# Kernel tuning notes

Measured on AMD Instinct MI355X. Metric: run time of the kernel, lower is better.

## Reference

```python
import jax, jax.numpy as jnp
import numpy as np

B, T, C, D = 8, 4096, 1024, 128  # batch, seq (=block_size), dim_embd, head_features

def setup_inputs() -> dict:
    key = jax.random.key(0)
    k1, k2, k3, k4 = jax.random.split(key, 4)
    s = 0.02
    return {
        "x": jax.random.normal(k1, (B, T, C), dtype=jnp.float32),
        "wq": jax.random.normal(k2, (C, D), dtype=jnp.float32) * s,
        "wk": jax.random.normal(k3, (C, D), dtype=jnp.float32) * s,
        "wv": jax.random.normal(k4, (C, D), dtype=jnp.float32) * s,
    }

def reference(x, wq, wk, wv):
    # q,k,v: [B,T,D]
    q = jnp.einsum('btc,cd->btd', x, wq)
    k = jnp.einsum('btc,cd->btd', x, wk)
    v = jnp.einsum('btc,cd->btd', x, wv)
    scale = k.shape[-1] ** -0.5
    wei = jnp.einsum('bqd,bkd->bqk', q, k) * scale  # [B,T,T]
    causal = jnp.tril(jnp.ones((T, T), dtype=bool))
    wei = jnp.where(causal, wei, -jnp.inf)
    attn = jax.nn.softmax(wei, axis=-1)  # dropout p=0.0 -> identity
    out = jnp.einsum('bqk,bkd->bqd', attn, v)  # [B,T,D]
    return out
```

## Files before the change

kernel.cpp:

```cpp
#include <hip/hip_runtime.h>

#define TT 4096
#define CC 1024
#define DD 128

typedef __attribute__((ext_vector_type(8))) short s16x8;
typedef __attribute__((ext_vector_type(4))) short s16x4;
typedef __attribute__((ext_vector_type(8))) __bf16 bf16x8;
typedef __attribute__((ext_vector_type(4))) float f32x4;
typedef __attribute__((ext_vector_type(2))) float f32x2;

__device__ __forceinline__ short f2bf(float f) {
    union { float f; unsigned u; } v; v.f = f;
    unsigned r = v.u + 0x7fffu + ((v.u >> 16) & 1u);
    return (short)(r >> 16);
}

__device__ __forceinline__ unsigned cvt_pk(float lo, float hi) {
    unsigned r;
    asm("v_cvt_pk_bf16_f32 %0, %1, %2" : "=v"(r) : "v"(lo), "v"(hi));
    return r;
}

__device__ __forceinline__ f32x4 mfma16(s16x8 a, s16x8 b, f32x4 c) {
    return __builtin_amdgcn_mfma_f32_16x16x32_bf16(
        __builtin_bit_cast(bf16x8, a), __builtin_bit_cast(bf16x8, b), c, 0, 0, 0);
}

__device__ __forceinline__ void gload_lds16(const short* g, short* l) {
    __builtin_amdgcn_global_load_lds(
        (const __attribute__((address_space(1))) void*)g,
        (__attribute__((address_space(3))) void*)l, 16, 0, 0);
}

__global__ void wt_kernel(const float* __restrict__ wq, const float* __restrict__ wk,
                          const float* __restrict__ wv, short* __restrict__ wT) {
    int idx = blockIdx.x * 256 + threadIdx.x;
    int d = idx & 127;
    int c = (idx >> 7) & 1023;
    int wsel = idx >> 17;
    const float* w = (wsel == 0) ? wq : (wsel == 1) ? wk : wv;
    float v = w[(size_t)c * DD + d];
    if (wsel == 0) v *= 0.08838834764831845f * 1.4426950408889634f;
    wT[(size_t)wsel * DD * CC + (size_t)d * CC + c] = f2bf(v);
}

__global__ __launch_bounds__(512)
void qkv_kernel(const float* __restrict__ x, const short* __restrict__ wT,
                short* __restrict__ qo, short* __restrict__ ko, short* __restrict__ vTo) {
    __shared__ short lw[2][384 * 64];
    const int mt = blockIdx.x;
    const int tid = threadIdx.x, lane = tid & 63, wid = tid >> 6;
    const int l15 = lane & 15, g = lane >> 4;
    const int wm = wid >> 1, wn = wid & 1;
    const int arow = mt * 128 + wm * 32 + l15;
    const float* xr0 = x + (size_t)arow * CC + g * 8;
    const float* xr1 = xr0 + (size_t)16 * CC;

    const f32x4 fz = {0.f, 0.f, 0.f, 0.f};
    f32x4 acc[2][12];
#pragma unroll
    for (int mr = 0; mr < 2; mr++)
#pragma unroll
        for (int nr = 0; nr < 12; nr++) acc[mr][nr] = fz;

    const int swr = wid * 48;
    const short* wsrc = wT + (size_t)(swr + (lane >> 3)) * CC + (lane & 7) * 8;

    float4 pa[2][2][2];
#define LOADA(kc) do { \
    _Pragma("unroll") for (int mr_ = 0; mr_ < 2; mr_++) \
    _Pragma("unroll") for (int ks_ = 0; ks_ < 2; ks_++) { \
        const float* p_ = (mr_ ? xr1 : xr0) + (kc) * 64 + ks_ * 32; \
        pa[mr_][ks_][0] = *(const float4*)p_; \
        pa[mr_][ks_][1] = *(const float4*)(p_ + 4); } \
} while (0)
#define STAGEW(kc, buf) do { \
    _Pragma("unroll") for (int j_ = 0; j_ < 6; j_++) \
        gload_lds16(wsrc + (size_t)(j_ * 8) * CC + (kc) * 64, &lw[buf][(swr + j_ * 8) * 64]); \
} while (0)

    LOADA(0);
    STAGEW(0, 0);
    asm volatile("s_waitcnt vmcnt(0)" ::: "memory");
    __builtin_amdgcn_s_barrier();
    int cur = 0;

    for (int kc = 0; kc < 16; kc++) {
        s16x8 af[2][2];
#pragma unroll
        for (int mr = 0; mr < 2; mr++)
#pragma unroll
            for (int ks = 0; ks < 2; ks++) {
                union { unsigned u[4]; s16x8 v; } cv;
                cv.u[0] = cvt_pk(pa[mr][ks][0].x, pa[mr][ks][0].y);
                cv.u[1] = cvt_pk(pa[mr][ks][0].z, pa[mr][ks][0].w);
                cv.u[2] = cvt_pk(pa[mr][ks][1].x, pa[mr][ks][1].y);
                cv.u[3] = cvt_pk(pa[mr][ks][1].z, pa[mr][ks][1].w);
                af[mr][ks] = cv.v;
            }
        if (kc < 15) { LOADA(kc + 1); STAGEW(kc + 1, cur ^ 1); }
        __builtin_amdgcn_s_setprio(1);
#pragma unroll
        for (int ks = 0; ks < 2; ks++)
#pragma unroll
            for (int nr = 0; nr < 12; nr++) {
                const s16x8 bfg = *(const s16x8*)
                    &lw[cur][(wn * 192 + nr * 16 + l15) * 64 + ks * 32 + g * 8];
                acc[0][nr] = mfma16(af[0][ks], bfg, acc[0][nr]);
                acc[1][nr] = mfma16(af[1][ks], bfg, acc[1][nr]);
            }
        __builtin_amdgcn_s_setprio(0);
        asm volatile("s_waitcnt vmcnt(0) lgkmcnt(0)" ::: "memory");
        __builtin_amdgcn_s_barrier();
        cur ^= 1;
    }

    const int bidx = mt >> 5;
    const int tb = (mt & 31) * 128 + wm * 32;
#pragma unroll
    for (int mr = 0; mr < 2; mr++)
#pragma unroll
        for (int nr = 0; nr < 12; nr++) {
            const int n = wn * 192 + nr * 16 + l15;
            if (n < 256) {
                short* dst; int d;
                if (n < 128) { dst = qo; d = n; } else { dst = ko; d = n - 128; }
#pragma unroll
                for (int i = 0; i < 4; i++) {
                    int t = tb + mr * 16 + g * 4 + i;
                    dst[((size_t)bidx * TT + t) * DD + d] = f2bf(acc[mr][nr][i]);
                }
            } else {
                const int d = n - 256;
                const int t = tb + mr * 16 + g * 4;
                uint2 u;
                u.x = cvt_pk(acc[mr][nr][0], acc[mr][nr][1]);
                u.y = cvt_pk(acc[mr][nr][2], acc[mr][nr][3]);
                *(uint2*)(vTo + ((size_t)bidx * DD + d) * TT + t) = u;
            }
        }
}

__device__ __forceinline__ void attn_stage(const short* kT, const short* vT, int kv0,
                                           short* lkb, short* lvb, int wid, int lane) {
#pragma unroll
    for (int j = 0; j < 4; j++) {
        int rbk = wid * 16 + j * 4;
        int rk = rbk + (lane >> 4);
        int ck = (lane & 15) ^ (rk & 7);
        gload_lds16(kT + (size_t)(kv0 + rk) * DD + ck * 8, lkb + rbk * 128);
        int rbv = wid * 32 + j * 8;
        int dv = rbv + (lane >> 3);
        int cv = (lane & 7) ^ (dv & 7);
        gload_lds16(vT + (size_t)dv * TT + kv0 + cv * 8, lvb + rbv * 64);
    }
}

__global__ __launch_bounds__(256)
void attn_kernel(const short* __restrict__ qb, const short* __restrict__ kb,
                 const short* __restrict__ vb, float* __restrict__ out,
                 float* __restrict__ opart, float* __restrict__ mlpart) {
    const int id = blockIdx.x;
    const int b  = id & 7;
    const int r3 = id >> 3;
    const int qt = r3 & 63;
    const int c  = r3 >> 6;
    const int t0 = c * 16;
    if (t0 > qt) return;
    const int t1 = (t0 + 16 < qt + 1) ? t0 + 16 : qt + 1;
    const int nc = (qt >> 4) + 1;

    __shared__ short lk[2][64 * 128];
    __shared__ short lv[2][128 * 64];
    __shared__ short lp[4][1024];
    const int tid = threadIdx.x, lane = tid & 63, wid = tid >> 6;
    const int l15 = lane & 15, g = lane >> 4;
    const int wq0 = qt * 64 + wid * 16;
    const short* kT = kb + (size_t)b * TT * DD;
    const short* vT = vb + (size_t)b * DD * TT;
    char* lpw = (char*)&lp[wid][0];
    const f32x4 fz = {0.f, 0.f, 0.f, 0.f};

    s16x8 qf[4];
    {
        const short* qp = qb + ((size_t)b * TT + wq0 + l15) * DD + g * 8;
#pragma unroll
        for (int ks = 0; ks < 4; ks++) qf[ks] = *(const s16x8*)(qp + ks * 32);
    }
    f32x4 o[8];
#pragma unroll
    for (int n = 0; n < 8; n++) o[n] = fz;
    float rmax = -1e30f, rsum = 0.f;

    attn_stage(kT, vT, t0 * 64, lk[0], lv[0], wid, lane);
    asm volatile("s_waitcnt vmcnt(0)" ::: "memory");
    __builtin_amdgcn_s_barrier();
    int cur = 0;

    for (int t = t0; t < t1; t++) {
        if (t + 1 < t1) attn_stage(kT, vT, (t + 1) * 64, lk[cur ^ 1], lv[cur ^ 1], wid, lane);
        const int kv0 = t * 64;
        const char* lkc = (const char*)&lk[cur][0];
        const char* lvc = (const char*)&lv[cur][0];

        f32x4 s[4];
        __builtin_amdgcn_s_setprio(1);
#pragma unroll
        for (int sub = 0; sub < 4; sub++) {
            f32x4 a = fz;
#pragma unroll
            for (int ks = 0; ks < 4; ks++) {
                int row = sub * 16 + l15;
                int byte = (row * 256 + ks * 64 + g * 16) ^ ((row & 7) << 4);
                s16x8 kf = *(const s16x8*)(lkc + byte);
                a = mfma16(kf, qf[ks], a);
            }
            s[sub] = a;
        }
        __builtin_amdgcn_s_setprio(0);
        if (t == qt) {
#pragma unroll
            for (int sub = 0; sub < 4; sub++)
#pragma unroll
                for (int i = 0; i < 4; i++) {
                    int k = kv0 + sub * 16 + 4 * g + i;
                    if (k > wq0 + l15) s[sub][i] = -1e30f;
                }
        }
        float m0 = s[0][0];
#pragma unroll
        for (int sub = 0; sub < 4; sub++)
#pragma unroll
            for (int i = 0; i < 4; i++) m0 = fmaxf(m0, s[sub][i]);
        m0 = fmaxf(m0, __shfl_xor(m0, 16));
        m0 = fmaxf(m0, __shfl_xor(m0, 32));
        float mnew = fmaxf(rmax, m0);
        float scal = exp2f(rmax - mnew);
        rmax = mnew;
        float ls = 0.f;
#pragma unroll
        for (int sub = 0; sub < 4; sub++)
#pragma unroll
            for (int i = 0; i < 4; i++) {
                float pv = exp2f(s[sub][i] - mnew);
                s[sub][i] = pv;
                ls += pv;
            }
        ls += __shfl_xor(ls, 16);
        ls += __shfl_xor(ls, 32);
        rsum = rsum * scal + ls;
#pragma unroll
        for (int sub = 0; sub < 4; sub++) {
            uint2 w01;
            w01.x = cvt_pk(s[sub][0], s[sub][1]);
            w01.y = cvt_pk(s[sub][2], s[sub][3]);
            int byte = (l15 * 128 + sub * 32 + g * 8) ^ ((l15 & 7) << 4);
            *(uint2*)(lpw + byte) = w01;
        }
#pragma unroll
        for (int n = 0; n < 8; n++)
#pragma unroll
            for (int i = 0; i < 4; i++) o[n][i] *= scal;
        __builtin_amdgcn_s_setprio(1);
#pragma unroll
        for (int ks2 = 0; ks2 < 2; ks2++) {
            int pbyte = (l15 * 128 + ks2 * 64 + g * 16) ^ ((l15 & 7) << 4);
            s16x8 pf = *(const s16x8*)(lpw + pbyte);
#pragma unroll
            for (int n = 0; n < 8; n++) {
                int vrow = n * 16 + l15;
                int vbyte = (vrow * 128 + ks2 * 64 + g * 16) ^ ((vrow & 7) << 4);
                s16x8 vf = *(const s16x8*)(lvc + vbyte);
                o[n] = mfma16(vf, pf, o[n]);
            }
        }
        __builtin_amdgcn_s_setprio(0);
        asm volatile("s_waitcnt vmcnt(0) lgkmcnt(0)" ::: "memory");
        __builtin_amdgcn_s_barrier();
        cur ^= 1;
    }

    const int r = wid * 16 + l15;
    if (nc == 1) {
        float inv = 1.0f / rsum;
        float* orow = out + ((size_t)b * TT + qt * 64 + r) * DD;
#pragma unroll
        for (int n = 0; n < 8; n++) {
            f32x4 w;
            w[0] = o[n][0] * inv; w[1] = o[n][1] * inv;
            w[2] = o[n][2] * inv; w[3] = o[n][3] * inv;
            __builtin_nontemporal_store(w, (f32x4*)(orow + n * 16 + 4 * g));
        }
    } else {
        const size_t pb = ((size_t)b * 48 + (qt - 16)) * 4 + c;
        float* prow = opart + pb * (64 * 128) + (size_t)r * 128;
#pragma unroll
        for (int n = 0; n < 8; n++) {
            __builtin_nontemporal_store(o[n], (f32x4*)(prow + n * 16 + 4 * g));
        }
        if (g == 0) {
            f32x2 s2; s2[0] = rmax; s2[1] = rsum;
            __builtin_nontemporal_store(s2, (f32x2*)(mlpart + (pb * 64 + r) * 2));
        }
    }
}

__global__ __launch_bounds__(256)
void comb_kernel(const float* __restrict__ opart, const float* __restrict__ mlpart,
                 float* __restrict__ out) {
    const int qtm = blockIdx.x;
    const int b = blockIdx.y;
    const int qt = 16 + qtm;
    const int nc = (qt >> 4) + 1;
    const int tid = threadIdx.x;
    const int row = tid >> 2, quad = tid & 3;
    const size_t base = ((size_t)b * 48 + qtm) * 4;

    float M = -3e38f;
    for (int cc = 0; cc < nc; cc++)
        M = fmaxf(M, mlpart[((base + cc) * 64 + row) * 2]);

    float acc[32];
#pragma unroll
    for (int k = 0; k < 32; k++) acc[k] = 0.f;
    float L = 0.f;
    for (int cc = 0; cc < nc; cc++) {
        float sm = mlpart[((base + cc) * 64 + row) * 2];
        float sl = mlpart[((base + cc) * 64 + row) * 2 + 1];
        float wgt = exp2f(sm - M);
        L += wgt * sl;
        const float* src = opart + (base + cc) * (64 * 128) + (size_t)row * 128 + quad * 32;
#pragma unroll
        for (int k = 0; k < 8; k++) {
            f32x4 v = __builtin_nontemporal_load((const f32x4*)(src + k * 4));
            acc[k * 4 + 0] += wgt * v[0];
            acc[k * 4 + 1] += wgt * v[1];
            acc[k * 4 + 2] += wgt * v[2];
            acc[k * 4 + 3] += wgt * v[3];
        }
    }
    float inv = 1.0f / L;
    float* dst = out + ((size_t)b * TT + qt * 64 + row) * DD + quad * 32;
#pragma unroll
    for (int k = 0; k < 8; k++) {
        f32x4 w;
        w[0] = acc[k * 4 + 0] * inv; w[1] = acc[k * 4 + 1] * inv;
        w[2] = acc[k * 4 + 2] * inv; w[3] = acc[k * 4 + 3] * inv;
        __builtin_nontemporal_store(w, (f32x4*)(dst + k * 4));
    }
}

extern "C" void kernel_launch(void* const* d_in, const int* in_sizes, int n_in,
                              void* d_out, int out_size, void* d_ws, size_t ws_size,
                              hipStream_t stream) {
    const float* x  = (const float*)d_in[0];
    const float* wq = (const float*)d_in[1];
    const float* wk = (const float*)d_in[2];
    const float* wv = (const float*)d_in[3];
    float* out = (float*)d_out;
    char* ws = (char*)d_ws;
    short* wT = (short*)ws;
    short* qb = (short*)(ws + 786432);
    short* kb = (short*)(ws + 786432 + 8388608);
    short* vb = (short*)(ws + 786432 + 16777216);
    float* opart = (float*)(ws + 786432 + 25165824);
    float* mlpart = (float*)(ws + 786432 + 25165824 + 50331648);

    wt_kernel<<<1536, 256, 0, stream>>>(wq, wk, wv, wT);
    qkv_kernel<<<256, 512, 0, stream>>>(x, wT, qb, kb, vb);
    attn_kernel<<<2048, 256, 0, stream>>>(qb, kb, vb, out, opart, mlpart);
    comb_kernel<<<dim3(48, 8), 256, 0, stream>>>(opart, mlpart, out);
}
```

Baseline: 195.4 us.

## Double query rows per attention block and single-buffer K/V with split-phase loads

```diff
diff --git a/kernel.cpp b/kernel.cpp
--- a/kernel.cpp
+++ b/kernel.cpp
@@ -142,166 +142,196 @@
         }
 }
 
-__device__ __forceinline__ void attn_stage(const short* kT, const short* vT, int kv0,
-                                           short* lkb, short* lvb, int wid, int lane) {
-#pragma unroll
-    for (int j = 0; j < 4; j++) {
-        int rbk = wid * 16 + j * 4;
-        int rk = rbk + (lane >> 4);
-        int ck = (lane & 15) ^ (rk & 7);
-        gload_lds16(kT + (size_t)(kv0 + rk) * DD + ck * 8, lkb + rbk * 128);
-        int rbv = wid * 32 + j * 8;
-        int dv = rbv + (lane >> 3);
-        int cv = (lane & 7) ^ (dv & 7);
-        gload_lds16(vT + (size_t)dv * TT + kv0 + cv * 8, lvb + rbv * 64);
-    }
-}
-
 __global__ __launch_bounds__(256)
 void attn_kernel(const short* __restrict__ qb, const short* __restrict__ kb,
                  const short* __restrict__ vb, float* __restrict__ out,
                  float* __restrict__ opart, float* __restrict__ mlpart) {
     const int id = blockIdx.x;
     const int b  = id & 7;
-    const int r3 = id >> 3;
-    const int qt = r3 & 63;
-    const int c  = r3 >> 6;
+    const int Q  = (id >> 3) & 31;
+    const int c  = id >> 8;
     const int t0 = c * 16;
-    if (t0 > qt) return;
-    const int t1 = (t0 + 16 < qt + 1) ? t0 + 16 : qt + 1;
-    const int nc = (qt >> 4) + 1;
-
-    __shared__ short lk[2][64 * 128];
-    __shared__ short lv[2][128 * 64];
-    __shared__ short lp[4][1024];
+    const int tend = 2 * Q + 2;
+    if (t0 >= tend) return;
+    const int t1 = (t0 + 16 < tend) ? t0 + 16 : tend;
+    const int nc = (tend + 15) >> 4;
+
+    __shared__ short lk[64 * 128];
+    __shared__ short lv[128 * 64];
+    __shared__ short lp[4][2048];
     const int tid = threadIdx.x, lane = tid & 63, wid = tid >> 6;
     const int l15 = lane & 15, g = lane >> 4;
-    const int wq0 = qt * 64 + wid * 16;
+    const int wq0 = Q * 128 + wid * 32;
+    const int tqw = wq0 >> 6;
     const short* kT = kb + (size_t)b * TT * DD;
     const short* vT = vb + (size_t)b * DD * TT;
     char* lpw = (char*)&lp[wid][0];
     const f32x4 fz = {0.f, 0.f, 0.f, 0.f};
 
-    s16x8 qf[4];
+    s16x8 qf0[4], qf1[4];
     {
-        const short* qp = qb + ((size_t)b * TT + wq0 + l15) * DD + g * 8;
-#pragma unroll
-        for (int ks = 0; ks < 4; ks++) qf[ks] = *(const s16x8*)(qp + ks * 32);
-    }
-    f32x4 o[8];
-#pragma unroll
-    for (int n = 0; n < 8; n++) o[n] = fz;
-    float rmax = -1e30f, rsum = 0.f;
-
-    attn_stage(kT, vT, t0 * 64, lk[0], lv[0], wid, lane);
+        const short* qp0 = qb + ((size_t)b * TT + wq0 + l15) * DD + g * 8;
+        const short* qp1 = qp0 + 16 * DD;
+#pragma unroll
+        for (int ks = 0; ks < 4; ks++) {
+            qf0[ks] = *(const s16x8*)(qp0 + ks * 32);
+            qf1[ks] = *(const s16x8*)(qp1 + ks * 32);
+        }
+    }
+    f32x4 o0[8], o1[8];
+#pragma unroll
+    for (int n = 0; n < 8; n++) { o0[n] = fz; o1[n] = fz; }
+    float rmax0 = -1e30f, rsum0 = 0.f, rmax1 = -1e30f, rsum1 = 0.f;
+
+#define SK(kv0) do { \
+    _Pragma("unroll") for (int j_ = 0; j_ < 4; j_++) { \
+        int rbk = wid * 16 + j_ * 4; \
+        int rk = rbk + (lane >> 4); \
+        int ck = (lane & 15) ^ (rk & 7); \
+        gload_lds16(kT + (size_t)((kv0) + rk) * DD + ck * 8, lk + rbk * 128); } \
+} while (0)
+#define SV(kv0) do { \
+    _Pragma("unroll") for (int j_ = 0; j_ < 4; j_++) { \
+        int rbv = wid * 32 + j_ * 8; \
+        int dv = rbv + (lane >> 3); \
+        int cv = (lane & 7) ^ (dv & 7); \
+        gload_lds16(vT + (size_t)dv * TT + (kv0) + cv * 8, lv + rbv * 64); } \
+} while (0)
+
+    SK(t0 * 64);
+    SV(t0 * 64);
     asm volatile("s_waitcnt vmcnt(0)" ::: "memory");
     __builtin_amdgcn_s_barrier();
-    int cur = 0;
 
     for (int t = t0; t < t1; t++) {
-        if (t + 1 < t1) attn_stage(kT, vT, (t + 1) * 64, lk[cur ^ 1], lv[cur ^ 1], wid, lane);
         const int kv0 = t * 64;
-        const char* lkc = (const char*)&lk[cur][0];
-        const char* lvc = (const char*)&lv[cur][0];
-
-        f32x4 s[4];
-        __builtin_amdgcn_s_setprio(1);
-#pragma unroll
-        for (int sub = 0; sub < 4; sub++) {
-            f32x4 a = fz;
-#pragma unroll
-            for (int ks = 0; ks < 4; ks++) {
-                int row = sub * 16 + l15;
-                int byte = (row * 256 + ks * 64 + g * 16) ^ ((row & 7) << 4);
-                s16x8 kf = *(const s16x8*)(lkc + byte);
-                a = mfma16(kf, qf[ks], a);
-            }
-            s[sub] = a;
-        }
-        __builtin_amdgcn_s_setprio(0);
-        if (t == qt) {
+        const int tn = (t + 1 < 63) ? t + 1 : 63;
+        asm volatile("s_waitcnt vmcnt(4)" ::: "memory");
+        f32x4 s0[4], s1[4];
+        if (t <= tqw) {
+            __builtin_amdgcn_s_setprio(1);
+#pragma unroll
+            for (int sub = 0; sub < 4; sub++) {
+                f32x4 a0 = fz, a1 = fz;
+#pragma unroll
+                for (int ks = 0; ks < 4; ks++) {
+                    int row = sub * 16 + l15;
+                    int byte = (row * 256 + ks * 64 + g * 16) ^ ((row & 7) << 4);
+                    s16x8 kf = *(const s16x8*)((const char*)lk + byte);
+                    a0 = mfma16(kf, qf0[ks], a0);
+                    a1 = mfma16(kf, qf1[ks], a1);
+                }
+                s0[sub] = a0; s1[sub] = a1;
+            }
+            __builtin_amdgcn_s_setprio(0);
+        }
+        __builtin_amdgcn_s_barrier();
+        SK(tn * 64);
+        if (t <= tqw) {
+            if (t == tqw) {
+#pragma unroll
+                for (int sub = 0; sub < 4; sub++)
+#pragma unroll
+                    for (int i = 0; i < 4; i++) {
+                        int k = kv0 + sub * 16 + 4 * g + i;
+                        if (k > wq0 + l15) s0[sub][i] = -1e30f;
+                        if (k > wq0 + 16 + l15) s1[sub][i] = -1e30f;
+                    }
+            }
+            float m0 = s0[0][0], m1 = s1[0][0];
 #pragma unroll
             for (int sub = 0; sub < 4; sub++)
 #pragma unroll
                 for (int i = 0; i < 4; i++) {
-                    int k = kv0 + sub * 16 + 4 * g + i;
-                    if (k > wq0 + l15) s[sub][i] = -1e30f;
+                    m0 = fmaxf(m0, s0[sub][i]);
+                    m1 = fmaxf(m1, s1[sub][i]);
                 }
-        }
-        float m0 = s[0][0];
-#pragma unroll
-        for (int sub = 0; sub < 4; sub++)
-#pragma unroll
-            for (int i = 0; i < 4; i++) m0 = fmaxf(m0, s[sub][i]);
-        m0 = fmaxf(m0, __shfl_xor(m0, 16));
-        m0 = fmaxf(m0, __shfl_xor(m0, 32));
-        float mnew = fmaxf(rmax, m0);
-        float scal = exp2f(rmax - mnew);
-        rmax = mnew;
-        float ls = 0.f;
-#pragma unroll
-        for (int sub = 0; sub < 4; sub++)
-#pragma unroll
-            for (int i = 0; i < 4; i++) {
-                float pv = exp2f(s[sub][i] - mnew);
-                s[sub][i] = pv;
-                ls += pv;
-            }
-        ls += __shfl_xor(ls, 16);
-        ls += __shfl_xor(ls, 32);
-        rsum = rsum * scal + ls;
-#pragma unroll
-        for (int sub = 0; sub < 4; sub++) {
-            uint2 w01;
-            w01.x = cvt_pk(s[sub][0], s[sub][1]);
-            w01.y = cvt_pk(s[sub][2], s[sub][3]);
-            int byte = (l15 * 128 + sub * 32 + g * 8) ^ ((l15 & 7) << 4);
-            *(uint2*)(lpw + byte) = w01;
-        }
-#pragma unroll
-        for (int n = 0; n < 8; n++)
-#pragma unroll
-            for (int i = 0; i < 4; i++) o[n][i] *= scal;
-        __builtin_amdgcn_s_setprio(1);
-#pragma unroll
-        for (int ks2 = 0; ks2 < 2; ks2++) {
-            int pbyte = (l15 * 128 + ks2 * 64 + g * 16) ^ ((l15 & 7) << 4);
-            s16x8 pf = *(const s16x8*)(lpw + pbyte);
+            m0 = fmaxf(m0, __shfl_xor(m0, 16));
+            m0 = fmaxf(m0, __shfl_xor(m0, 32));
+            m1 = fmaxf(m1, __shfl_xor(m1, 16));
+            m1 = fmaxf(m1, __shfl_xor(m1, 32));
+            float mn0 = fmaxf(rmax0, m0), mn1 = fmaxf(rmax1, m1);
+            float sc0 = exp2f(rmax0 - mn0), sc1 = exp2f(rmax1 - mn1);
+            rmax0 = mn0; rmax1 = mn1;
+            float ls0 = 0.f, ls1 = 0.f;
+#pragma unroll
+            for (int sub = 0; sub < 4; sub++)
+#pragma unroll
+                for (int i = 0; i < 4; i++) {
+                    float p0 = exp2f(s0[sub][i] - mn0);
+                    float p1 = exp2f(s1[sub][i] - mn1);
+                    s0[sub][i] = p0; s1[sub][i] = p1;
+                    ls0 += p0; ls1 += p1;
+                }
+            ls0 += __shfl_xor(ls0, 16); ls0 += __shfl_xor(ls0, 32);
+            ls1 += __shfl_xor(ls1, 16); ls1 += __shfl_xor(ls1, 32);
+            rsum0 = rsum0 * sc0 + ls0;
+            rsum1 = rsum1 * sc1 + ls1;
+#pragma unroll
+            for (int sub = 0; sub < 4; sub++) {
+                uint2 w0, w1;
+                w0.x = cvt_pk(s0[sub][0], s0[sub][1]);
+                w0.y = cvt_pk(s0[sub][2], s0[sub][3]);
+                w1.x = cvt_pk(s1[sub][0], s1[sub][1]);
+                w1.y = cvt_pk(s1[sub][2], s1[sub][3]);
+                int byte = (l15 * 128 + sub * 32 + g * 8) ^ ((l15 & 7) << 4);
+                *(uint2*)(lpw + byte) = w0;
+                *(uint2*)(lpw + 2048 + byte) = w1;
+            }
+#pragma unroll
+            for (int n = 0; n < 8; n++)
+#pragma unroll
+                for (int i = 0; i < 4; i++) { o0[n][i] *= sc0; o1[n][i] *= sc1; }
+        }
+        asm volatile("s_waitcnt vmcnt(4)" ::: "memory");
+        if (t <= tqw) {
+            __builtin_amdgcn_s_setprio(1);
+#pragma unroll
+            for (int ks2 = 0; ks2 < 2; ks2++) {
+                int pbyte = (l15 * 128 + ks2 * 64 + g * 16) ^ ((l15 & 7) << 4);
+                s16x8 pf0 = *(const s16x8*)(lpw + pbyte);
+                s16x8 pf1 = *(const s16x8*)(lpw + 2048 + pbyte);
+#pragma unroll
+                for (int n = 0; n < 8; n++) {
+                    int vrow = n * 16 + l15;
+                    int vbyte = (vrow * 128 + ks2 * 64 + g * 16) ^ ((vrow & 7) << 4);
+                    s16x8 vf = *(const s16x8*)((const char*)lv + vbyte);
+                    o0[n] = mfma16(vf, pf0, o0[n]);
+                    o1[n] = mfma16(vf, pf1, o1[n]);
+                }
+            }
+            __builtin_amdgcn_s_setprio(0);
+        }
+        __builtin_amdgcn_s_barrier();
+        SV(tn * 64);
+    }
+
+#pragma unroll
+    for (int h = 0; h < 2; h++) {
+        const int r = wid * 32 + h * 16 + l15;
+        const float rs = h ? rsum1 : rsum0;
+        const float rm = h ? rmax1 : rmax0;
+        const f32x4* oo = h ? o1 : o0;
+        if (nc == 1) {
+            float inv = 1.0f / rs;
+            float* orow = out + ((size_t)b * TT + Q * 128 + r) * DD;
 #pragma unroll
             for (int n = 0; n < 8; n++) {
-                int vrow = n * 16 + l15;
-                int vbyte = (vrow * 128 + ks2 * 64 + g * 16) ^ ((vrow & 7) << 4);
-                s16x8 vf = *(const s16x8*)(lvc + vbyte);
-                o[n] = mfma16(vf, pf, o[n]);
-            }
-        }
-        __builtin_amdgcn_s_setprio(0);
-        asm volatile("s_waitcnt vmcnt(0) lgkmcnt(0)" ::: "memory");
-        __builtin_amdgcn_s_barrier();
-        cur ^= 1;
-    }
-
-    const int r = wid * 16 + l15;
-    if (nc == 1) {
-        float inv = 1.0f / rsum;
-        float* orow = out + ((size_t)b * TT + qt * 64 + r) * DD;
-#pragma unroll
-        for (int n = 0; n < 8; n++) {
-            f32x4 w;
-            w[0] = o[n][0] * inv; w[1] = o[n][1] * inv;
-            w[2] = o[n][2] * inv; w[3] = o[n][3] * inv;
-            __builtin_nontemporal_store(w, (f32x4*)(orow + n * 16 + 4 * g));
-        }
-    } else {
-        const size_t pb = ((size_t)b * 48 + (qt - 16)) * 4 + c;
-        float* prow = opart + pb * (64 * 128) + (size_t)r * 128;
-#pragma unroll
-        for (int n = 0; n < 8; n++) {
-            __builtin_nontemporal_store(o[n], (f32x4*)(prow + n * 16 + 4 * g));
-        }
-        if (g == 0) {
-            f32x2 s2; s2[0] = rmax; s2[1] = rsum;
-            __builtin_nontemporal_store(s2, (f32x2*)(mlpart + (pb * 64 + r) * 2));
+                f32x4 w;
+                w[0] = oo[n][0] * inv; w[1] = oo[n][1] * inv;
+                w[2] = oo[n][2] * inv; w[3] = oo[n][3] * inv;
+                __builtin_nontemporal_store(w, (f32x4*)(orow + n * 16 + 4 * g));
+            }
+        } else {
+            const size_t pb = ((size_t)b * 24 + (Q - 8)) * 4 + c;
+            float* prow = opart + pb * (128 * 128) + (size_t)r * 128;
+#pragma unroll
+            for (int n = 0; n < 8; n++)
+                __builtin_nontemporal_store(oo[n], (f32x4*)(prow + n * 16 + 4 * g));
+            if (g == 0) {
+                f32x2 s2; s2[0] = rm; s2[1] = rs;
+                __builtin_nontemporal_store(s2, (f32x2*)(mlpart + (pb * 128 + r) * 2));
+            }
         }
     }
 }
@@ -309,28 +339,28 @@
 __global__ __launch_bounds__(256)
 void comb_kernel(const float* __restrict__ opart, const float* __restrict__ mlpart,
                  float* __restrict__ out) {
-    const int qtm = blockIdx.x;
+    const int qh = blockIdx.x;
     const int b = blockIdx.y;
-    const int qt = 16 + qtm;
-    const int nc = (qt >> 4) + 1;
+    const int Q = 8 + (qh >> 1);
+    const int nc = (2 * Q + 2 + 15) >> 4;
     const int tid = threadIdx.x;
-    const int row = tid >> 2, quad = tid & 3;
-    const size_t base = ((size_t)b * 48 + qtm) * 4;
+    const int r = (qh & 1) * 64 + (tid >> 2), quad = tid & 3;
+    const size_t base = ((size_t)b * 24 + (Q - 8)) * 4;
 
     float M = -3e38f;
     for (int cc = 0; cc < nc; cc++)
-        M = fmaxf(M, mlpart[((base + cc) * 64 + row) * 2]);
+        M = fmaxf(M, mlpart[((base + cc) * 128 + r) * 2]);
 
     float acc[32];
 #pragma unroll
     for (int k = 0; k < 32; k++) acc[k] = 0.f;
     float L = 0.f;
     for (int cc = 0; cc < nc; cc++) {
-        float sm = mlpart[((base + cc) * 64 + row) * 2];
-        float sl = mlpart[((base + cc) * 64 + row) * 2 + 1];
+        float sm = mlpart[((base + cc) * 128 + r) * 2];
+        float sl = mlpart[((base + cc) * 128 + r) * 2 + 1];
         float wgt = exp2f(sm - M);
         L += wgt * sl;
-        const float* src = opart + (base + cc) * (64 * 128) + (size_t)row * 128 + quad * 32;
+        const float* src = opart + (base + cc) * (128 * 128) + (size_t)r * 128 + quad * 32;
 #pragma unroll
         for (int k = 0; k < 8; k++) {
             f32x4 v = __builtin_nontemporal_load((const f32x4*)(src + k * 4));
@@ -341,7 +371,7 @@
         }
     }
     float inv = 1.0f / L;
-    float* dst = out + ((size_t)b * TT + qt * 64 + row) * DD + quad * 32;
+    float* dst = out + ((size_t)b * TT + Q * 128 + r) * DD + quad * 32;
 #pragma unroll
     for (int k = 0; k < 8; k++) {
         f32x4 w;
@@ -369,6 +399,6 @@
 
     wt_kernel<<<1536, 256, 0, stream>>>(wq, wk, wv, wT);
     qkv_kernel<<<256, 512, 0, stream>>>(x, wT, qb, kb, vb);
-    attn_kernel<<<2048, 256, 0, stream>>>(qb, kb, vb, out, opart, mlpart);
+    attn_kernel<<<1024, 256, 0, stream>>>(qb, kb, vb, out, opart, mlpart);
     comb_kernel<<<dim3(48, 8), 256, 0, stream>>>(opart, mlpart, out);
 }
```

New measurement: 231.9 us. 18.7% more time.

## Fuse split-KV combine into attention via atomic last-block and shrink QKV k-chunk

Applied to the files above, without the earlier changes.

```diff
diff --git a/kernel.cpp b/kernel.cpp
--- a/kernel.cpp
+++ b/kernel.cpp
@@ -48,7 +48,7 @@
 __global__ __launch_bounds__(512)
 void qkv_kernel(const float* __restrict__ x, const short* __restrict__ wT,
                 short* __restrict__ qo, short* __restrict__ ko, short* __restrict__ vTo) {
-    __shared__ short lw[2][384 * 64];
+    __shared__ short lw[2][384 * 32];
     const int mt = blockIdx.x;
     const int tid = threadIdx.x, lane = tid & 63, wid = tid >> 6;
     const int l15 = lane & 15, g = lane >> 4;
@@ -65,19 +65,18 @@
         for (int nr = 0; nr < 12; nr++) acc[mr][nr] = fz;
 
     const int swr = wid * 48;
-    const short* wsrc = wT + (size_t)(swr + (lane >> 3)) * CC + (lane & 7) * 8;
-
-    float4 pa[2][2][2];
+    const short* wsrc = wT + (size_t)(swr + (lane >> 2)) * CC + (lane & 3) * 8;
+
+    float4 pa[2][2];
 #define LOADA(kc) do { \
-    _Pragma("unroll") for (int mr_ = 0; mr_ < 2; mr_++) \
-    _Pragma("unroll") for (int ks_ = 0; ks_ < 2; ks_++) { \
-        const float* p_ = (mr_ ? xr1 : xr0) + (kc) * 64 + ks_ * 32; \
-        pa[mr_][ks_][0] = *(const float4*)p_; \
-        pa[mr_][ks_][1] = *(const float4*)(p_ + 4); } \
+    _Pragma("unroll") for (int mr_ = 0; mr_ < 2; mr_++) { \
+        const float* p_ = (mr_ ? xr1 : xr0) + (kc) * 32; \
+        pa[mr_][0] = *(const float4*)p_; \
+        pa[mr_][1] = *(const float4*)(p_ + 4); } \
 } while (0)
 #define STAGEW(kc, buf) do { \
-    _Pragma("unroll") for (int j_ = 0; j_ < 6; j_++) \
-        gload_lds16(wsrc + (size_t)(j_ * 8) * CC + (kc) * 64, &lw[buf][(swr + j_ * 8) * 64]); \
+    _Pragma("unroll") for (int j_ = 0; j_ < 3; j_++) \
+        gload_lds16(wsrc + (size_t)(j_ * 16) * CC + (kc) * 32, &lw[buf][(swr + j_ * 16) * 32]); \
 } while (0)
 
     LOADA(0);
@@ -86,30 +85,26 @@
     __builtin_amdgcn_s_barrier();
     int cur = 0;
 
-    for (int kc = 0; kc < 16; kc++) {
-        s16x8 af[2][2];
-#pragma unroll
-        for (int mr = 0; mr < 2; mr++)
-#pragma unroll
-            for (int ks = 0; ks < 2; ks++) {
-                union { unsigned u[4]; s16x8 v; } cv;
-                cv.u[0] = cvt_pk(pa[mr][ks][0].x, pa[mr][ks][0].y);
-                cv.u[1] = cvt_pk(pa[mr][ks][0].z, pa[mr][ks][0].w);
-                cv.u[2] = cvt_pk(pa[mr][ks][1].x, pa[mr][ks][1].y);
-                cv.u[3] = cvt_pk(pa[mr][ks][1].z, pa[mr][ks][1].w);
-                af[mr][ks] = cv.v;
-            }
-        if (kc < 15) { LOADA(kc + 1); STAGEW(kc + 1, cur ^ 1); }
+    for (int kc = 0; kc < 32; kc++) {
+        s16x8 af[2];
+#pragma unroll
+        for (int mr = 0; mr < 2; mr++) {
+            union { unsigned u[4]; s16x8 v; } cv;
+            cv.u[0] = cvt_pk(pa[mr][0].x, pa[mr][0].y);
+            cv.u[1] = cvt_pk(pa[mr][0].z, pa[mr][0].w);
+            cv.u[2] = cvt_pk(pa[mr][1].x, pa[mr][1].y);
+            cv.u[3] = cvt_pk(pa[mr][1].z, pa[mr][1].w);
+            af[mr] = cv.v;
+        }
+        if (kc < 31) { LOADA(kc + 1); STAGEW(kc + 1, cur ^ 1); }
         __builtin_amdgcn_s_setprio(1);
 #pragma unroll
-        for (int ks = 0; ks < 2; ks++)
-#pragma unroll
-            for (int nr = 0; nr < 12; nr++) {
-                const s16x8 bfg = *(const s16x8*)
-                    &lw[cur][(wn * 192 + nr * 16 + l15) * 64 + ks * 32 + g * 8];
-                acc[0][nr] = mfma16(af[0][ks], bfg, acc[0][nr]);
-                acc[1][nr] = mfma16(af[1][ks], bfg, acc[1][nr]);
-            }
+        for (int nr = 0; nr < 12; nr++) {
+            const s16x8 bfg = *(const s16x8*)
+                &lw[cur][(wn * 192 + nr * 16 + l15) * 32 + g * 8];
+            acc[0][nr] = mfma16(af[0], bfg, acc[0][nr]);
+            acc[1][nr] = mfma16(af[1], bfg, acc[1][nr]);
+        }
         __builtin_amdgcn_s_setprio(0);
         asm volatile("s_waitcnt vmcnt(0) lgkmcnt(0)" ::: "memory");
         __builtin_amdgcn_s_barrier();
@@ -160,7 +155,8 @@
 __global__ __launch_bounds__(256)
 void attn_kernel(const short* __restrict__ qb, const short* __restrict__ kb,
                  const short* __restrict__ vb, float* __restrict__ out,
-                 float* __restrict__ opart, float* __restrict__ mlpart) {
+                 float* __restrict__ opart, float* __restrict__ mlpart,
+                 int* __restrict__ ctr) {
     const int id = blockIdx.x;
     const int b  = id & 7;
     const int r3 = id >> 3;
@@ -174,6 +170,7 @@
     __shared__ short lk[2][64 * 128];
     __shared__ short lv[2][128 * 64];
     __shared__ short lp[4][1024];
+    __shared__ int lastFlag;
     const int tid = threadIdx.x, lane = tid & 63, wid = tid >> 6;
     const int l15 = lane & 15, g = lane >> 4;
     const int wq0 = qt * 64 + wid * 16;
@@ -292,62 +289,62 @@
             w[2] = o[n][2] * inv; w[3] = o[n][3] * inv;
             __builtin_nontemporal_store(w, (f32x4*)(orow + n * 16 + 4 * g));
         }
-    } else {
-        const size_t pb = ((size_t)b * 48 + (qt - 16)) * 4 + c;
+        return;
+    }
+    const size_t pb = ((size_t)b * 48 + (qt - 16)) * 4 + c;
+    {
         float* prow = opart + pb * (64 * 128) + (size_t)r * 128;
 #pragma unroll
-        for (int n = 0; n < 8; n++) {
+        for (int n = 0; n < 8; n++)
             __builtin_nontemporal_store(o[n], (f32x4*)(prow + n * 16 + 4 * g));
-        }
         if (g == 0) {
             f32x2 s2; s2[0] = rmax; s2[1] = rsum;
             __builtin_nontemporal_store(s2, (f32x2*)(mlpart + (pb * 64 + r) * 2));
         }
     }
-}
-
-__global__ __launch_bounds__(256)
-void comb_kernel(const float* __restrict__ opart, const float* __restrict__ mlpart,
-                 float* __restrict__ out) {
-    const int qtm = blockIdx.x;
-    const int b = blockIdx.y;
-    const int qt = 16 + qtm;
-    const int nc = (qt >> 4) + 1;
-    const int tid = threadIdx.x;
-    const int row = tid >> 2, quad = tid & 3;
-    const size_t base = ((size_t)b * 48 + qtm) * 4;
-
-    float M = -3e38f;
-    for (int cc = 0; cc < nc; cc++)
-        M = fmaxf(M, mlpart[((base + cc) * 64 + row) * 2]);
-
-    float acc[32];
-#pragma unroll
-    for (int k = 0; k < 32; k++) acc[k] = 0.f;
-    float L = 0.f;
-    for (int cc = 0; cc < nc; cc++) {
-        float sm = mlpart[((base + cc) * 64 + row) * 2];
-        float sl = mlpart[((base + cc) * 64 + row) * 2 + 1];
-        float wgt = exp2f(sm - M);
-        L += wgt * sl;
-        const float* src = opart + (base + cc) * (64 * 128) + (size_t)row * 128 + quad * 32;
+    __threadfence();
+    __syncthreads();
+    if (tid == 0) {
+        int old = atomicAdd(&ctr[b * 48 + (qt - 16)], 1);
+        lastFlag = (old == nc - 1);
+    }
+    __syncthreads();
+    if (!lastFlag) return;
+    __threadfence();
+    {
+        const int row = tid >> 2, quad = tid & 3;
+        const size_t base = ((size_t)b * 48 + (qt - 16)) * 4;
+        float M = -3e38f;
+        for (int cc = 0; cc < nc; cc++)
+            M = fmaxf(M, mlpart[((base + cc) * 64 + row) * 2]);
+        float acc[32];
+#pragma unroll
+        for (int k = 0; k < 32; k++) acc[k] = 0.f;
+        float L = 0.f;
+        for (int cc = 0; cc < nc; cc++) {
+            float sm = mlpart[((base + cc) * 64 + row) * 2];
+            float sl = mlpart[((base + cc) * 64 + row) * 2 + 1];
+            float wgt = exp2f(sm - M);
+            L += wgt * sl;
+            const float* src = opart + (base + cc) * (64 * 128) + (size_t)row * 128 + quad * 32;
+#pragma unroll
+            for (int k = 0; k < 8; k++) {
+                f32x4 v = __builtin_nontemporal_load((const f32x4*)(src + k * 4));
+                acc[k * 4 + 0] += wgt * v[0];
+                acc[k * 4 + 1] += wgt * v[1];
+                acc[k * 4 + 2] += wgt * v[2];
+                acc[k * 4 + 3] += wgt * v[3];
+            }
+        }
+        float inv = 1.0f / L;
+        float* dst = out + ((size_t)b * TT + qt * 64 + row) * DD + quad * 32;
 #pragma unroll
         for (int k = 0; k < 8; k++) {
-            f32x4 v = __builtin_nontemporal_load((const f32x4*)(src + k * 4));
-            acc[k * 4 + 0] += wgt * v[0];
-            acc[k * 4 + 1] += wgt * v[1];
-            acc[k * 4 + 2] += wgt * v[2];
-            acc[k * 4 + 3] += wgt * v[3];
-        }
-    }
-    float inv = 1.0f / L;
-    float* dst = out + ((size_t)b * TT + qt * 64 + row) * DD + quad * 32;
-#pragma unroll
-    for (int k = 0; k < 8; k++) {
-        f32x4 w;
-        w[0] = acc[k * 4 + 0] * inv; w[1] = acc[k * 4 + 1] * inv;
-        w[2] = acc[k * 4 + 2] * inv; w[3] = acc[k * 4 + 3] * inv;
-        __builtin_nontemporal_store(w, (f32x4*)(dst + k * 4));
+            f32x4 w;
+            w[0] = acc[k * 4 + 0] * inv; w[1] = acc[k * 4 + 1] * inv;
+            w[2] = acc[k * 4 + 2] * inv; w[3] = acc[k * 4 + 3] * inv;
+            __builtin_nontemporal_store(w, (f32x4*)(dst + k * 4));
+        }
     }
 }
 
@@ -366,9 +363,10 @@
     short* vb = (short*)(ws + 786432 + 16777216);
     float* opart = (float*)(ws + 786432 + 25165824);
     float* mlpart = (float*)(ws + 786432 + 25165824 + 50331648);
-
+    int* ctr = (int*)(ws + 786432 + 25165824 + 50331648 + 786432);
+
+    hipMemsetAsync(ctr, 0, 384 * sizeof(int), stream);
     wt_kernel<<<1536, 256, 0, stream>>>(wq, wk, wv, wT);
     qkv_kernel<<<256, 512, 0, stream>>>(x, wT, qb, kb, vb);
-    attn_kernel<<<2048, 256, 0, stream>>>(qb, kb, vb, out, opart, mlpart);
-    comb_kernel<<<dim3(48, 8), 256, 0, stream>>>(opart, mlpart, out);
-}
+    attn_kernel<<<2048, 256, 0, stream>>>(qb, kb, vb, out, opart, mlpart, ctr);
+}
```

Result: slower. 422.6 us (+116.2%).
